# Kernel tuning notes

Hardware: AMD Instinct MI355X
Metric: run time of the kernel (lower is better)

Reference implementation:

```python
import jax, jax.numpy as jnp
import numpy as np

N_NODES = 50000


def gcn_conv(x, row, col, ew, W, b):
    # PyG GCNConv with edge_weight: add self-loops (weight 1), symmetric norm,
    # then scatter-add of normalized messages at target nodes.
    n = x.shape[0]
    loop = jnp.arange(n)
    row_f = jnp.concatenate([row, loop])
    col_f = jnp.concatenate([col, loop])
    w_f = jnp.concatenate([ew, jnp.ones((n,), dtype=x.dtype)])
    deg = jax.ops.segment_sum(w_f, col_f, num_segments=n)  # [N]
    dinv = jnp.where(deg > 0, jax.lax.rsqrt(deg), jnp.zeros_like(deg))
    norm = dinv[row_f] * w_f * dinv[col_f]                 # [E+N]
    h = x @ W                                              # [N, out]
    msgs = h[row_f] * norm[:, None]                        # gather + weight
    out = jax.ops.segment_sum(msgs, col_f, num_segments=n) # scatter_add
    return out + b


def setup_inputs() -> dict:
    key = jax.random.key(0)
    ks = jax.random.split(key, 12)
    E = 1600000
    nf, ef, efil, nfil, classes = 128, 16, 32, 128, 40
    x = jax.random.normal(ks[0], (N_NODES, nf), dtype=jnp.float32)
    edge_index = jax.random.randint(ks[1], (2, E), 0, N_NODES, dtype=jnp.int64)
    edge_x = jax.random.normal(ks[2], (E, ef), dtype=jnp.float32)
    def lin(k, fan_in, shape):
        bound = 1.0 / np.sqrt(fan_in)
        return jax.random.uniform(k, shape, jnp.float32, -bound, bound)
    W1 = lin(ks[3], ef, (ef, efil)); b1 = lin(ks[4], ef, (efil,))
    W2 = lin(ks[5], efil, (efil, 1)); b2 = lin(ks[6], efil, (1,))
    Wg1 = lin(ks[7], nf, (nf, nfil)); bg1 = jnp.zeros((nfil,), jnp.float32)
    Wg2 = lin(ks[8], nfil, (nfil, classes)); bg2 = jnp.zeros((classes,), jnp.float32)
    return {"x": x, "edge_index": edge_index, "edge_x": edge_x,
            "W1": W1, "b1": b1, "W2": W2, "b2": b2,
            "Wg1": Wg1, "bg1": bg1, "Wg2": Wg2, "bg2": bg2}


def reference(x, edge_index, edge_x, W1, b1, W2, b2, Wg1, bg1, Wg2, bg2):
    row, col = edge_index[0], edge_index[1]
    # edge-weight MLP: relu -> sigmoid scalar per edge
    e = jax.nn.relu(edge_x @ W1 + b1)
    ew = jax.nn.sigmoid(e @ W2 + b2).reshape(-1)  # [E]
    h = gcn_conv(x, row, col, ew, Wg1, bg1)
    h = jax.nn.relu(h)
    # F.dropout(training=self.training): identity at inference
    out = gcn_conv(h, row, col, ew, Wg2, bg2)
    return out
```

## Files before the change

### kernel.cpp

```cpp
#include <hip/hip_runtime.h>
#include <hip/hip_bf16.h>
#include <math.h>


#define NF   128
#define EF   16
#define EFIL 32
#define NCLS 40
#define TILE 4096

__device__ inline unsigned pack_bf16x2(float a, float b) {
    unsigned ua = __float_as_uint(a);
    unsigned ub = __float_as_uint(b);
    ua += 0x7FFF + ((ua >> 16) & 1);
    ub += 0x7FFF + ((ub >> 16) & 1);
    return (ua >> 16) | (ub & 0xFFFF0000u);
}
__device__ inline float bf16_lo(unsigned u) { return __uint_as_float(u << 16); }
__device__ inline float bf16_hi(unsigned u) { return __uint_as_float(u & 0xFFFF0000u); }

__global__ __launch_bounds__(256) void edge_mlp_kernel(
    const float* __restrict__ ex, const float* __restrict__ W1,
    const float* __restrict__ b1, const float* __restrict__ W2,
    const float* __restrict__ b2, float* __restrict__ ew, int E)
{
    __shared__ float sW1[EF * EFIL];
    __shared__ float sb1[EFIL];
    __shared__ float sW2[EFIL];
    __shared__ float sb2;
    int t = threadIdx.x;
    for (int i = t; i < EF * EFIL; i += 256) sW1[i] = W1[i];
    if (t < EFIL) { sb1[t] = b1[t]; sW2[t] = W2[t]; }
    if (t == 0) sb2 = b2[0];
    __syncthreads();

    int e = blockIdx.x * 256 + t;
    if (e >= E) return;

    float xv[EF];
    const float4* exv = (const float4*)(ex) + (size_t)e * (EF / 4);
    #pragma unroll
    for (int q = 0; q < EF / 4; q++) {
        float4 v = exv[q];
        xv[q * 4 + 0] = v.x; xv[q * 4 + 1] = v.y;
        xv[q * 4 + 2] = v.z; xv[q * 4 + 3] = v.w;
    }
    float acc = sb2;
    #pragma unroll
    for (int j = 0; j < EFIL; j++) {
        float h = sb1[j];
        #pragma unroll
        for (int k = 0; k < EF; k++) h += xv[k] * sW1[k * EFIL + j];
        acc += fmaxf(h, 0.0f) * sW2[j];
    }
    ew[e] = 1.0f / (1.0f + expf(-acc));
}

__global__ __launch_bounds__(256) void hist1_kernel(
    const int* __restrict__ col, int* __restrict__ hist, int E, int ntiles)
{
    __shared__ int h[256];
    int t = threadIdx.x;
    h[t] = 0;
    __syncthreads();
    int tile = blockIdx.x;
    int base = tile * TILE;
    int end = base + TILE; if (end > E) end = E;
    for (int i = base + t; i < end; i += 256)
        atomicAdd(&h[col[i] >> 8], 1);
    __syncthreads();
    hist[t * ntiles + tile] = h[t];
}

__global__ __launch_bounds__(256) void scanA_kernel(
    int* __restrict__ hist, int* __restrict__ dtot, int ntiles)
{
    __shared__ int ts[256];
    int d = blockIdx.x;
    int t = threadIdx.x;
    int* hrow = hist + (size_t)d * ntiles;
    int C = (ntiles + 255) >> 8;
    int b = t * C;
    int e = b + C; if (e > ntiles) e = ntiles;
    int s = 0;
    for (int i = b; i < e; i++) s += hrow[i];
    ts[t] = s;
    __syncthreads();
    for (int dd = 1; dd < 256; dd <<= 1) {
        int v = (t >= dd) ? ts[t - dd] : 0;
        __syncthreads();
        ts[t] += v;
        __syncthreads();
    }
    int run = ts[t] - s;
    for (int i = b; i < e; i++) {
        int v = hrow[i];
        hrow[i] = run;
        run += v;
    }
    if (t == 255) dtot[d] = ts[255];
}

__global__ __launch_bounds__(256) void scanB_kernel(
    const int* __restrict__ dtot, int* __restrict__ dbase, int E)
{
    __shared__ int ts[256];
    int t = threadIdx.x;
    int s = dtot[t];
    ts[t] = s;
    __syncthreads();
    for (int dd = 1; dd < 256; dd <<= 1) {
        int v = (t >= dd) ? ts[t - dd] : 0;
        __syncthreads();
        ts[t] += v;
        __syncthreads();
    }
    dbase[t] = ts[t] - s;
    if (t == 255) dbase[256] = E;
}

__global__ __launch_bounds__(512) void scatter1_kernel(
    const int* __restrict__ row, const int* __restrict__ col,
    const float* __restrict__ ew, const int* __restrict__ hscan,
    const int* __restrict__ dbase,
    uint4* __restrict__ st, int E, int ntiles)
{
    __shared__ int cur[256];
    int t = threadIdx.x;
    int tile = blockIdx.x;
    if (t < 256) cur[t] = dbase[t] + hscan[t * ntiles + tile];
    __syncthreads();
    int base = tile * TILE;
    int end = base + TILE; if (end > E) end = E;
    for (int i = base + t; i < end; i += 512) {
        int c = col[i];
        int r = row[i];
        float w = ew[i];
        int p = atomicAdd(&cur[c >> 8], 1);
        st[p] = make_uint4((unsigned)c, (unsigned)r, __float_as_uint(w), 0u);
    }
}

__global__ __launch_bounds__(512) void bucket_sort_kernel(
    const uint4* __restrict__ st, const int* __restrict__ dbase,
    uint2* __restrict__ edgeF, int* __restrict__ offs, float* __restrict__ dinv,
    int E, int N)
{
    __shared__ int   cnt[256];
    __shared__ int   scan[256];
    __shared__ int   cursor[256];
    __shared__ float dsum[256];
    __shared__ float sdinv[256];
    int t = threadIdx.x;
    int b = blockIdx.x;
    if (t == 0 && b == 0) offs[N] = E;
    int bstart = dbase[b];
    int bend   = dbase[b + 1];
    if (t < 256) { cnt[t] = 0; dsum[t] = 0.0f; sdinv[t] = 0.0f; }
    __syncthreads();
    for (int i = bstart + t; i < bend; i += 512) {
        uint4 v = st[i];
        int lo = (int)(v.x & 255u);
        atomicAdd(&cnt[lo], 1);
        atomicAdd(&dsum[lo], __uint_as_float(v.z));
    }
    __syncthreads();
    if (t < 256) scan[t] = cnt[t];
    __syncthreads();
    for (int d = 1; d < 256; d <<= 1) {
        int v = 0;
        if (t < 256 && t >= d) v = scan[t - d];
        __syncthreads();
        if (t < 256) scan[t] += v;
        __syncthreads();
    }
    if (t < 256) {
        int excl = scan[t] - cnt[t];
        int c = (b << 8) + t;
        cursor[t] = bstart + excl;
        if (c < N) {
            offs[c] = bstart + excl;
            float deg = 1.0f + dsum[t];
            float di = rsqrtf(deg);
            sdinv[t] = di;
            dinv[c] = di;
        }
    }
    __syncthreads();
    for (int i = bstart + t; i < bend; i += 512) {
        uint4 v = st[i];
        int lo = (int)(v.x & 255u);
        int p = atomicAdd(&cursor[lo], 1);
        float w = __uint_as_float(v.z) * sdinv[lo];
        edgeF[p] = make_uint2(v.y, __float_as_uint(w));
    }
}

#define G1_ROWS 64
#define XPAD 68
__global__ __launch_bounds__(256, 4) void gemm1_kernel(
    const float* __restrict__ x, const float* __restrict__ W,
    const float* __restrict__ dinv, unsigned short* __restrict__ h1b, int N)
{
    __shared__ float sx[NF * XPAD];
    int t = threadIdx.x;
    int row0 = blockIdx.x * G1_ROWS;
    for (int i = t; i < G1_ROWS * NF; i += 256) {
        int r = i >> 7, k = i & 127;
        int gr = row0 + r;
        sx[k * XPAD + r] = (gr < N) ? x[(size_t)gr * NF + k] : 0.0f;
    }
    __syncthreads();

    int fg = t & 31, rg = t >> 5;
    int f0 = fg * 4, r0 = rg * 8;
    float acc[8][4];
    #pragma unroll
    for (int r = 0; r < 8; r++)
        #pragma unroll
        for (int c = 0; c < 4; c++) acc[r][c] = 0.0f;

    #pragma unroll 8
    for (int k = 0; k < NF; k++) {
        float4 w  = *(const float4*)&W[(size_t)k * NF + f0];
        float4 xa = *(const float4*)&sx[k * XPAD + r0];
        float4 xb = *(const float4*)&sx[k * XPAD + r0 + 4];
        float xr[8] = {xa.x, xa.y, xa.z, xa.w, xb.x, xb.y, xb.z, xb.w};
        #pragma unroll
        for (int r = 0; r < 8; r++) {
            acc[r][0] += xr[r] * w.x;
            acc[r][1] += xr[r] * w.y;
            acc[r][2] += xr[r] * w.z;
            acc[r][3] += xr[r] * w.w;
        }
    }
    #pragma unroll
    for (int r = 0; r < 8; r++) {
        int gr = row0 + r0 + r;
        if (gr < N) {
            float di = dinv[gr];
            uint2 p;
            p.x = pack_bf16x2(acc[r][0] * di, acc[r][1] * di);
            p.y = pack_bf16x2(acc[r][2] * di, acc[r][3] * di);
            *(uint2*)(h1b + (size_t)gr * NF + f0) = p;
        }
    }
}

__global__ __launch_bounds__(256) void gather1_kernel(
    const int* __restrict__ offs, const uint2* __restrict__ edgeF,
    const unsigned short* __restrict__ h1b,
    const float* __restrict__ dinv, const float* __restrict__ bg1,
    float* __restrict__ out1, int N)
{
    int wid  = threadIdx.x >> 6;
    int lane = threadIdx.x & 63;
    int c = blockIdx.x * 4 + wid;
    if (c >= N) return;
    float di = dinv[c];
    unsigned hu = *(const unsigned*)(h1b + (size_t)c * NF + 2 * lane);
    float2 acc;
    acc.x = bg1[2 * lane]     + bf16_lo(hu) * di;
    acc.y = bg1[2 * lane + 1] + bf16_hi(hu) * di;

    int beg = offs[c], end = offs[c + 1];
    for (int e0 = beg; e0 < end; e0 += 64) {
        int idx = e0 + lane;
        uint2 eg = make_uint2(0u, 0u);
        if (idx < end) eg = edgeF[idx];
        int sv = (int)eg.x; float wv = __uint_as_float(eg.y);
        int m = end - e0; if (m > 64) m = 64;
        int j = 0;
        for (; j + 8 <= m; j += 8) {
            unsigned v[8]; float w[8];
            #pragma unroll
            for (int u = 0; u < 8; u++) {
                int s = __shfl(sv, j + u);
                w[u] = __shfl(wv, j + u);
                v[u] = *(const unsigned*)(h1b + (size_t)s * NF + 2 * lane);
            }
            #pragma unroll
            for (int u = 0; u < 8; u++) {
                acc.x += w[u] * bf16_lo(v[u]);
                acc.y += w[u] * bf16_hi(v[u]);
            }
        }
        for (; j < m; j++) {
            int   s = __shfl(sv, j);
            float w = __shfl(wv, j);
            unsigned v = *(const unsigned*)(h1b + (size_t)s * NF + 2 * lane);
            acc.x += w * bf16_lo(v);
            acc.y += w * bf16_hi(v);
        }
    }
    *(float2*)(out1 + (size_t)c * NF + 2 * lane) = acc;
}

#define G2_ROWS 64
__global__ __launch_bounds__(256, 4) void gemm2_kernel(
    const float* __restrict__ out1, const float* __restrict__ W,
    const float* __restrict__ dinv, unsigned short* __restrict__ h2b, int N)
{
    __shared__ float sx[NF * XPAD];
    int t = threadIdx.x;
    int row0 = blockIdx.x * G2_ROWS;
    for (int i = t; i < G2_ROWS * NF; i += 256) {
        int r = i >> 7, k = i & 127;
        int gr = row0 + r;
        sx[k * XPAD + r] = (gr < N) ? fmaxf(out1[(size_t)gr * NF + k], 0.0f) : 0.0f;
    }
    __syncthreads();

    int fg = t & 15, rg = t >> 4;
    int f0 = fg * 4;
    int f0c = (f0 <= NCLS - 4) ? f0 : (NCLS - 4);
    int r0 = rg * 4;
    float acc[4][4];
    #pragma unroll
    for (int r = 0; r < 4; r++)
        #pragma unroll
        for (int c = 0; c < 4; c++) acc[r][c] = 0.0f;

    #pragma unroll 8
    for (int k = 0; k < NF; k++) {
        float4 w  = *(const float4*)&W[(size_t)k * NCLS + f0c];
        float4 xa = *(const float4*)&sx[k * XPAD + r0];
        float xr[4] = {xa.x, xa.y, xa.z, xa.w};
        #pragma unroll
        for (int r = 0; r < 4; r++) {
            acc[r][0] += xr[r] * w.x;
            acc[r][1] += xr[r] * w.y;
            acc[r][2] += xr[r] * w.z;
            acc[r][3] += xr[r] * w.w;
        }
    }
    if (f0 <= NCLS - 4) {
        #pragma unroll
        for (int r = 0; r < 4; r++) {
            int gr = row0 + r0 + r;
            if (gr < N) {
                float di = dinv[gr];
                uint2 p;
                p.x = pack_bf16x2(acc[r][0] * di, acc[r][1] * di);
                p.y = pack_bf16x2(acc[r][2] * di, acc[r][3] * di);
                *(uint2*)(h2b + (size_t)gr * NCLS + f0) = p;
            }
        }
    }
}

__global__ __launch_bounds__(256) void gather2_kernel(
    const int* __restrict__ offs, const uint2* __restrict__ edgeF,
    const unsigned short* __restrict__ h2b,
    const float* __restrict__ dinv, const float* __restrict__ bg2,
    float* __restrict__ out, int N)
{
    int wid  = threadIdx.x >> 6;
    int lane = threadIdx.x & 63;
    int c = blockIdx.x * 4 + wid;
    if (c >= N) return;
    float di = dinv[c];
    float2 acc = {0.0f, 0.0f};
    if (lane < NCLS / 2) {
        unsigned hu = *(const unsigned*)(h2b + (size_t)c * NCLS + 2 * lane);
        acc.x = bg2[2 * lane]     + bf16_lo(hu) * di;
        acc.y = bg2[2 * lane + 1] + bf16_hi(hu) * di;
    }

    int beg = offs[c], end = offs[c + 1];
    for (int e0 = beg; e0 < end; e0 += 64) {
        int idx = e0 + lane;
        uint2 eg = make_uint2(0u, 0u);
        if (idx < end) eg = edgeF[idx];
        int sv = (int)eg.x; float wv = __uint_as_float(eg.y);
        int m = end - e0; if (m > 64) m = 64;
        int j = 0;
        for (; j + 8 <= m; j += 8) {
            unsigned v[8]; float w[8];
            #pragma unroll
            for (int u = 0; u < 8; u++) {
                int s = __shfl(sv, j + u);
                w[u] = __shfl(wv, j + u);
                v[u] = (lane < NCLS / 2)
                     ? *(const unsigned*)(h2b + (size_t)s * NCLS + 2 * lane) : 0u;
            }
            #pragma unroll
            for (int u = 0; u < 8; u++) {
                acc.x += w[u] * bf16_lo(v[u]);
                acc.y += w[u] * bf16_hi(v[u]);
            }
        }
        for (; j < m; j++) {
            int   s = __shfl(sv, j);
            float w = __shfl(wv, j);
            if (lane < NCLS / 2) {
                unsigned v = *(const unsigned*)(h2b + (size_t)s * NCLS + 2 * lane);
                acc.x += w * bf16_lo(v);
                acc.y += w * bf16_hi(v);
            }
        }
    }
    if (lane < NCLS / 2) *(float2*)(out + (size_t)c * NCLS + 2 * lane) = acc;
}

extern "C" void kernel_launch(void* const* d_in, const int* in_sizes, int n_in,
                              void* d_out, int out_size, void* d_ws, size_t ws_size,
                              hipStream_t stream)
{
    const float* x   = (const float*)d_in[0];
    const int*   ei  = (const int*)d_in[1];
    const float* exf = (const float*)d_in[2];
    const float* W1  = (const float*)d_in[3];
    const float* b1  = (const float*)d_in[4];
    const float* W2  = (const float*)d_in[5];
    const float* b2  = (const float*)d_in[6];
    const float* Wg1 = (const float*)d_in[7];
    const float* bg1 = (const float*)d_in[8];
    const float* Wg2 = (const float*)d_in[9];
    const float* bg2 = (const float*)d_in[10];
    float* out = (float*)d_out;

    int N = in_sizes[0] / NF;
    int E = in_sizes[2] / EF;
    const int* row = ei;
    const int* col = ei + E;
    int ntiles = (E + TILE - 1) / TILE;
    int L = 256 * ntiles;

    char* base = (char*)d_ws;
    size_t off = 0;
    auto alloc = [&](size_t words) -> void* {
        void* p = base + off * 4;
        off += (words + 3) & ~(size_t)3;
        return p;
    };
    float* ew   = (float*)alloc(E);
    size_t stwords = (size_t)4 * E;
    size_t hwords = ((size_t)N * NF + 1) / 2;
    if (hwords > stwords) stwords = hwords;
    uint4* st   = (uint4*)alloc(stwords);
    unsigned short* h1b = (unsigned short*)st;
    unsigned short* h2b = (unsigned short*)st;
    uint2* edgeF = (uint2*)alloc((size_t)2 * E);
    float* out1 = (float*)alloc((size_t)N * NF);
    float* dinv = (float*)alloc(N);
    int*   offs = (int*)  alloc(N + 1);
    int*   hist = (int*)  alloc(L);
    int*   dtot = (int*)  alloc(256);
    int*   dbase= (int*)  alloc(257);

    int nb;
    nb = (E + 255) / 256;
    edge_mlp_kernel<<<nb, 256, 0, stream>>>(exf, W1, b1, W2, b2, ew, E);

    hist1_kernel<<<ntiles, 256, 0, stream>>>(col, hist, E, ntiles);
    scanA_kernel<<<256, 256, 0, stream>>>(hist, dtot, ntiles);
    scanB_kernel<<<1, 256, 0, stream>>>(dtot, dbase, E);
    scatter1_kernel<<<ntiles, 512, 0, stream>>>(row, col, ew, hist, dbase,
                                                st, E, ntiles);
    bucket_sort_kernel<<<256, 512, 0, stream>>>(st, dbase, edgeF, offs, dinv, E, N);

    nb = (N + G1_ROWS - 1) / G1_ROWS;
    gemm1_kernel<<<nb, 256, 0, stream>>>(x, Wg1, dinv, h1b, N);

    nb = (N + 3) / 4;
    gather1_kernel<<<nb, 256, 0, stream>>>(offs, edgeF, h1b, dinv, bg1, out1, N);

    nb = (N + G2_ROWS - 1) / G2_ROWS;
    gemm2_kernel<<<nb, 256, 0, stream>>>(out1, Wg2, dinv, h2b, N);

    nb = (N + 3) / 4;
    gather2_kernel<<<nb, 256, 0, stream>>>(offs, edgeF, h2b, dinv, bg2, out, N);
}
```

Before: 432.6 us.

## Fuse edge MLP into scatter kernel and pack scatter records to 8 bytes

The separate edge-MLP kernel is removed and the sigmoid edge weight is computed inside the scatter pass, so the per-edge weight array is never written to or read back from global memory. The scatter record shrinks from 16 to 8 bytes by packing the source row and the low 8 bits of the target into one word, which halves traffic in the scatter and in both bucket-sort passes. The scatter kernel now does the MLP arithmetic with only ntiles blocks (about 391) of 512 threads, so it has less parallelism than the old per-edge launch. The packing needs row < 2^24, which holds for 50000 nodes.

```diff
diff --git a/kernel.cpp b/kernel.cpp
--- a/kernel.cpp
+++ b/kernel.cpp
@@ -18,43 +18,6 @@
 }
 __device__ inline float bf16_lo(unsigned u) { return __uint_as_float(u << 16); }
 __device__ inline float bf16_hi(unsigned u) { return __uint_as_float(u & 0xFFFF0000u); }
-
-__global__ __launch_bounds__(256) void edge_mlp_kernel(
-    const float* __restrict__ ex, const float* __restrict__ W1,
-    const float* __restrict__ b1, const float* __restrict__ W2,
-    const float* __restrict__ b2, float* __restrict__ ew, int E)
-{
-    __shared__ float sW1[EF * EFIL];
-    __shared__ float sb1[EFIL];
-    __shared__ float sW2[EFIL];
-    __shared__ float sb2;
-    int t = threadIdx.x;
-    for (int i = t; i < EF * EFIL; i += 256) sW1[i] = W1[i];
-    if (t < EFIL) { sb1[t] = b1[t]; sW2[t] = W2[t]; }
-    if (t == 0) sb2 = b2[0];
-    __syncthreads();
-
-    int e = blockIdx.x * 256 + t;
-    if (e >= E) return;
-
-    float xv[EF];
-    const float4* exv = (const float4*)(ex) + (size_t)e * (EF / 4);
-    #pragma unroll
-    for (int q = 0; q < EF / 4; q++) {
-        float4 v = exv[q];
-        xv[q * 4 + 0] = v.x; xv[q * 4 + 1] = v.y;
-        xv[q * 4 + 2] = v.z; xv[q * 4 + 3] = v.w;
-    }
-    float acc = sb2;
-    #pragma unroll
-    for (int j = 0; j < EFIL; j++) {
-        float h = sb1[j];
-        #pragma unroll
-        for (int k = 0; k < EF; k++) h += xv[k] * sW1[k * EFIL + j];
-        acc += fmaxf(h, 0.0f) * sW2[j];
-    }
-    ew[e] = 1.0f / (1.0f + expf(-acc));
-}
 
 __global__ __launch_bounds__(256) void hist1_kernel(
     const int* __restrict__ col, int* __restrict__ hist, int E, int ntiles)
@@ -119,30 +82,57 @@
     if (t == 255) dbase[256] = E;
 }
 
-__global__ __launch_bounds__(512) void scatter1_kernel(
+__global__ __launch_bounds__(512) void scatter_mlp_kernel(
+    const float* __restrict__ ex, const float* __restrict__ W1,
+    const float* __restrict__ b1, const float* __restrict__ W2,
+    const float* __restrict__ b2,
     const int* __restrict__ row, const int* __restrict__ col,
-    const float* __restrict__ ew, const int* __restrict__ hscan,
-    const int* __restrict__ dbase,
-    uint4* __restrict__ st, int E, int ntiles)
-{
+    const int* __restrict__ hscan, const int* __restrict__ dbase,
+    uint2* __restrict__ st, int E, int ntiles)
+{
+    __shared__ float sW1[EF * EFIL];
+    __shared__ float sb1[EFIL];
+    __shared__ float sW2[EFIL];
+    __shared__ float sb2;
     __shared__ int cur[256];
     int t = threadIdx.x;
     int tile = blockIdx.x;
+    for (int i = t; i < EF * EFIL; i += 512) sW1[i] = W1[i];
+    if (t < EFIL) { sb1[t] = b1[t]; sW2[t] = W2[t]; }
+    if (t == 0) sb2 = b2[0];
     if (t < 256) cur[t] = dbase[t] + hscan[t * ntiles + tile];
     __syncthreads();
+
     int base = tile * TILE;
     int end = base + TILE; if (end > E) end = E;
     for (int i = base + t; i < end; i += 512) {
+        float xv[EF];
+        const float4* exv = (const float4*)(ex) + (size_t)i * (EF / 4);
+        #pragma unroll
+        for (int q = 0; q < EF / 4; q++) {
+            float4 v = exv[q];
+            xv[q * 4 + 0] = v.x; xv[q * 4 + 1] = v.y;
+            xv[q * 4 + 2] = v.z; xv[q * 4 + 3] = v.w;
+        }
+        float acc = sb2;
+        #pragma unroll
+        for (int j = 0; j < EFIL; j++) {
+            float h = sb1[j];
+            #pragma unroll
+            for (int k = 0; k < EF; k++) h += xv[k] * sW1[k * EFIL + j];
+            acc += fmaxf(h, 0.0f) * sW2[j];
+        }
+        float s = 1.0f / (1.0f + expf(-acc));
         int c = col[i];
         int r = row[i];
-        float w = ew[i];
         int p = atomicAdd(&cur[c >> 8], 1);
-        st[p] = make_uint4((unsigned)c, (unsigned)r, __float_as_uint(w), 0u);
+        st[p] = make_uint2(((unsigned)r << 8) | (unsigned)(c & 255),
+                           __float_as_uint(s));
     }
 }
 
 __global__ __launch_bounds__(512) void bucket_sort_kernel(
-    const uint4* __restrict__ st, const int* __restrict__ dbase,
+    const uint2* __restrict__ st, const int* __restrict__ dbase,
     uint2* __restrict__ edgeF, int* __restrict__ offs, float* __restrict__ dinv,
     int E, int N)
 {
@@ -159,10 +149,10 @@
     if (t < 256) { cnt[t] = 0; dsum[t] = 0.0f; sdinv[t] = 0.0f; }
     __syncthreads();
     for (int i = bstart + t; i < bend; i += 512) {
-        uint4 v = st[i];
+        uint2 v = st[i];
         int lo = (int)(v.x & 255u);
         atomicAdd(&cnt[lo], 1);
-        atomicAdd(&dsum[lo], __uint_as_float(v.z));
+        atomicAdd(&dsum[lo], __uint_as_float(v.y));
     }
     __syncthreads();
     if (t < 256) scan[t] = cnt[t];
@@ -188,11 +178,11 @@
     }
     __syncthreads();
     for (int i = bstart + t; i < bend; i += 512) {
-        uint4 v = st[i];
+        uint2 v = st[i];
         int lo = (int)(v.x & 255u);
         int p = atomicAdd(&cursor[lo], 1);
-        float w = __uint_as_float(v.z) * sdinv[lo];
-        edgeF[p] = make_uint2(v.y, __float_as_uint(w));
+        float w = __uint_as_float(v.y) * sdinv[lo];
+        edgeF[p] = make_uint2(v.x >> 8, __float_as_uint(w));
     }
 }
 
@@ -434,11 +424,10 @@
         off += (words + 3) & ~(size_t)3;
         return p;
     };
-    float* ew   = (float*)alloc(E);
-    size_t stwords = (size_t)4 * E;
+    size_t stwords = (size_t)2 * E;
     size_t hwords = ((size_t)N * NF + 1) / 2;
     if (hwords > stwords) stwords = hwords;
-    uint4* st   = (uint4*)alloc(stwords);
+    uint2* st   = (uint2*)alloc(stwords);
     unsigned short* h1b = (unsigned short*)st;
     unsigned short* h2b = (unsigned short*)st;
     uint2* edgeF = (uint2*)alloc((size_t)2 * E);
@@ -450,14 +439,12 @@
     int*   dbase= (int*)  alloc(257);
 
     int nb;
-    nb = (E + 255) / 256;
-    edge_mlp_kernel<<<nb, 256, 0, stream>>>(exf, W1, b1, W2, b2, ew, E);
-
     hist1_kernel<<<ntiles, 256, 0, stream>>>(col, hist, E, ntiles);
     scanA_kernel<<<256, 256, 0, stream>>>(hist, dtot, ntiles);
     scanB_kernel<<<1, 256, 0, stream>>>(dtot, dbase, E);
-    scatter1_kernel<<<ntiles, 512, 0, stream>>>(row, col, ew, hist, dbase,
-                                                st, E, ntiles);
+    scatter_mlp_kernel<<<ntiles, 512, 0, stream>>>(exf, W1, b1, W2, b2,
+                                                   row, col, hist, dbase,
+                                                   st, E, ntiles);
     bucket_sort_kernel<<<256, 512, 0, stream>>>(st, dbase, edgeF, offs, dinv, E, N);
 
     nb = (N + G1_ROWS - 1) / G1_ROWS;
```

After: 593.7 us. 37.2% more time.
